# Kernel optimization log

Measured on AMD Instinct MI355X. Metric: run time of the kernel, lower is better.

The kernel has to match this reference:

```python
import jax, jax.numpy as jnp
import numpy as np

L, d, D, X, B = 64, 2, 32, 2, 2048  # sites, local dim, bond dim, kraus dim, batch
STD = 0.01  # kernel_init = normal(stddev=0.01)


def setup_inputs() -> dict:
    key = jax.random.key(0)
    k1, k2, k3, k4 = jax.random.split(key, 4)
    # local quantum-number indices for (row, col) halves: shape [B, 2L]
    qn = jax.random.randint(k1, (B, 2 * L), 0, d, dtype=jnp.int32)
    # boundary tensors: random + all-ones boundary (as in setup())
    left = STD * jax.random.normal(k2, (d, D, X), jnp.float32) + jnp.ones((d, D, X), jnp.float32)
    right = STD * jax.random.normal(k3, (d, D, X), jnp.float32) + jnp.ones((d, D, X), jnp.float32)
    # middle tensors: random + identity on the (D,D) bond indices for every (site, s, kraus)
    iden = jnp.broadcast_to(jnp.eye(D, dtype=jnp.float32)[None, None, :, :, None], (L - 2, d, D, D, X))
    middle = STD * jax.random.normal(k4, (L - 2, d, D, D, X), jnp.float32) + iden
    return {"qn": qn, "left_tensors": left, "right_tensors": right, "middle_tensors": middle}


def _contract_mpdo(qn, left_tensors, right_tensors, middle_tensors):
    # qn: [2L] ints; split into row / column quantum numbers of the density matrix
    qn_r, qn_c = jnp.split(qn, 2, axis=-1)
    # left/right boundary edges: (D,X) @ (X,D) -> (D,D)
    left_edge = left_tensors[qn_r[0]] @ jnp.conj(left_tensors[qn_c[0]]).T
    right_edge = right_tensors[qn_r[-1]] @ jnp.conj(right_tensors[qn_c[-1]]).T

    @jax.checkpoint
    def step(edge, pair):
        tensor, sr, sc = pair  # tensor: (d,D,D,X)
        # (D,D,X) x (D,D) -> (D,X,D)
        tri = jnp.einsum('ijk,il->jkl', tensor[sr], edge)
        # (D,X,D) x (D,D,X) -> (D,D)
        new_edge = jnp.einsum('jkl,lmk->jm', tri, jnp.conj(tensor[sc]))
        return new_edge, None

    edge, _ = jax.lax.scan(step, left_edge, (middle_tensors, qn_r[1:-1], qn_c[1:-1]), unroll=1)
    return jnp.einsum('ij,ij->', edge, right_edge)


def reference(qn, left_tensors, right_tensors, middle_tensors):
    rho = jax.vmap(lambda q: _contract_mpdo(q, left_tensors, right_tensors, middle_tensors))(qn)
    return jnp.log(rho.astype(jnp.complex64))
```

## Files before the change

### kernel.cpp

```cpp
#include <hip/hip_runtime.h>
#include <hip/hip_bf16.h>
#include <math.h>


typedef __attribute__((ext_vector_type(8)))  short short8;
typedef __attribute__((ext_vector_type(16))) float f32x16;

#define EPITCH 33

static __device__ inline unsigned pk2(float lo, float hi) {
    union { __hip_bfloat162 h; unsigned u; } cv;
    cv.h = __float22bfloat162_rn(make_float2(lo, hi));
    return cv.u;
}
static __device__ inline short8 mk8(unsigned u0, unsigned u1, unsigned u2, unsigned u3) {
    union { short8 v; unsigned u[4]; } r;
    r.u[0] = u0; r.u[1] = u1; r.u[2] = u2; r.u[3] = u3;
    return r.v;
}
static __device__ inline void pl32swap(unsigned& x, unsigned& y) {
    asm("v_permlane32_swap_b32 %0, %1" : "+v"(x), "+v"(y));
}
static __device__ inline f32x16 MFMA(short8 a, short8 b, f32x16 c) {
    return __builtin_amdgcn_mfma_f32_32x32x16_bf16(a, b, c, 0, 0, 0);
}
static __device__ inline f32x16 zero16() {
    f32x16 z = {0.f,0.f,0.f,0.f,0.f,0.f,0.f,0.f,0.f,0.f,0.f,0.f,0.f,0.f,0.f,0.f};
    return z;
}

__global__ __launch_bounds__(256, 2) void mpdo_mfma(
    const int*   __restrict__ qn,
    const float* __restrict__ left,
    const float* __restrict__ right,
    const float* __restrict__ middle,
    float*       __restrict__ out,
    const int    cplx)
{
    __shared__ unsigned mid_b[2048];
    __shared__ float    E_s[4][32*EPITCH];

    const int t    = threadIdx.x;
    const int w    = t >> 6;
    const int lane = t & 63;
    const int hi   = lane >> 5;
    const int col  = lane & 31;
    const int elem = blockIdx.x * 4 + w;
    const int* q   = qn + (size_t)elem * 128;
    float* Ew = E_s[w];

    const int sp = (t >> 4) & 15;
    const int sj = t & 15;
    const int jj = sj * 2;
    const float dj = (sp == sj) ? 1.0f : 0.0f;
    const int v0 = (0 + 2*sp) * 16 + sj;
    const int v1 = (32 + 2*sp) * 16 + sj;

    int rowr[16];
    #pragma unroll
    for (int r = 0; r < 16; ++r) rowr[r] = (r & 3) + 8*(r >> 2) + 4*hi;

    float e[16];
    {
        const float* Lr = left + (size_t)q[0]  * 64;
        const float* Lc = left + (size_t)q[64] * 64;
        const float c0v = Lc[col*2 + 0], c1v = Lc[col*2 + 1];
        #pragma unroll
        for (int r = 0; r < 16; ++r)
            e[r] = Lr[rowr[r]*2 + 0] * c0v + Lr[rowr[r]*2 + 1] * c1v;
    }

    const float4* gm = (const float4*)middle;
    float4 A0 = gm[v0], A1 = gm[v0 + 16], B0 = gm[v1], B1 = gm[v1 + 16];
    int srn = q[1], scn = q[65];

    for (int site = 1; site <= 62; ++site) {
        {
            uint2* m2 = (uint2*)mid_b;
            m2[((0*16 + sp)*32 + jj) >> 1] = make_uint2(pk2(A0.x - dj, A1.x), pk2(A0.z, A1.z - dj));
            m2[((1*16 + sp)*32 + jj) >> 1] = make_uint2(pk2(A0.y - dj, A1.y), pk2(A0.w, A1.w - dj));
            m2[((2*16 + sp)*32 + jj) >> 1] = make_uint2(pk2(B0.x - dj, B1.x), pk2(B0.z, B1.z - dj));
            m2[((3*16 + sp)*32 + jj) >> 1] = make_uint2(pk2(B0.y - dj, B1.y), pk2(B0.w, B1.w - dj));
        }
        #pragma unroll
        for (int r = 0; r < 16; ++r) Ew[rowr[r]*EPITCH + col] = e[r];
        __syncthreads();

        const int sr = srn, sc = scn;
        if (site < 62) {
            const float4* gn = (const float4*)(middle + (size_t)site * 4096);
            A0 = gn[v0]; A1 = gn[v0 + 16]; B0 = gn[v1]; B1 = gn[v1 + 16];
            srn = q[site + 1]; scn = q[site + 65];
        }

        short8 aT[2][2], bF[2][2];
        #pragma unroll
        for (int k = 0; k < 2; ++k) {
            #pragma unroll
            for (int h = 0; h < 2; ++h) {
                const int pa = ((sr*2 + k)*16 + 8*h + 4*hi) * 32 + col;
                aT[k][h] = mk8(mid_b[pa], mid_b[pa+32], mid_b[pa+64], mid_b[pa+96]);
                const int pb = ((sc*2 + k)*16 + 8*h + 4*hi) * 32 + col;
                bF[k][h] = mk8(mid_b[pb], mid_b[pb+32], mid_b[pb+64], mid_b[pb+96]);
            }
        }
        short8 EA[2];
        #pragma unroll
        for (int h = 0; h < 2; ++h) {
            const int base = col*EPITCH + 16*h + 8*hi;
            const float f0 = Ew[base+0], f1 = Ew[base+1], f2 = Ew[base+2], f3 = Ew[base+3];
            const float f4 = Ew[base+4], f5 = Ew[base+5], f6 = Ew[base+6], f7 = Ew[base+7];
            EA[h] = mk8(pk2(f0,f1), pk2(f2,f3), pk2(f4,f5), pk2(f6,f7));
        }
        short8 EB[2];
        #pragma unroll
        for (int h = 0; h < 2; ++h) {
            unsigned ua = pk2(e[8*h+0], e[8*h+1]);
            unsigned ub = pk2(e[8*h+2], e[8*h+3]);
            unsigned uc = pk2(e[8*h+4], e[8*h+5]);
            unsigned ud = pk2(e[8*h+6], e[8*h+7]);
            pl32swap(ua, uc); pl32swap(ub, ud);
            EB[h] = mk8(ua, ub, uc, ud);
        }

        f32x16 V0 = MFMA(EA[0], bF[0][0], zero16());
        V0 = MFMA(EA[1], bF[0][1], V0);
        f32x16 V1 = MFMA(EA[0], bF[1][0], zero16());
        V1 = MFMA(EA[1], bF[1][1], V1);
        f32x16 acc = MFMA(aT[0][0], EB[0], zero16());
        acc = MFMA(aT[0][1], EB[1], acc);
        acc = MFMA(aT[1][0], EB[0], acc);
        acc = MFMA(aT[1][1], EB[1], acc);
        #pragma unroll
        for (int k = 0; k < 2; ++k) {
            const f32x16& V = k ? V1 : V0;
            #pragma unroll
            for (int h = 0; h < 2; ++h) {
                unsigned ua = pk2(V[8*h+0], V[8*h+1]);
                unsigned ub = pk2(V[8*h+2], V[8*h+3]);
                unsigned uc = pk2(V[8*h+4], V[8*h+5]);
                unsigned ud = pk2(V[8*h+6], V[8*h+7]);
                pl32swap(ua, uc); pl32swap(ub, ud);
                acc = MFMA(aT[k][h], mk8(ua, ub, uc, ud), acc);
            }
        }
        #pragma unroll
        for (int r = 0; r < 16; ++r)
            e[r] = 2.0f*e[r] + acc[r] + V0[r] + V1[r];
        __syncthreads();
    }

    {
        const float* Rr = right + (size_t)q[63]  * 64;
        const float* Rc = right + (size_t)q[127] * 64;
        const float rc0 = Rc[col*2 + 0], rc1 = Rc[col*2 + 1];
        float part = 0.f;
        #pragma unroll
        for (int r = 0; r < 16; ++r) {
            const float re = Rr[rowr[r]*2 + 0]*rc0 + Rr[rowr[r]*2 + 1]*rc1;
            part += e[r] * re;
        }
        #pragma unroll
        for (int off = 32; off > 0; off >>= 1)
            part += __shfl_down(part, off, 64);
        if (lane == 0) {
            const float re = logf(fabsf(part));
            if (cplx) {
                out[2*elem + 0] = re;
                out[2*elem + 1] = (part < 0.f) ? 3.14159265358979323846f : 0.f;
            } else {
                out[elem] = re;
            }
        }
    }
}

extern "C" void kernel_launch(void* const* d_in, const int* in_sizes, int n_in,
                              void* d_out, int out_size, void* d_ws, size_t ws_size,
                              hipStream_t stream) {
    const int*   qn     = (const int*)  d_in[0];
    const float* left   = (const float*)d_in[1];
    const float* right  = (const float*)d_in[2];
    const float* middle = (const float*)d_in[3];
    float* out = (float*)d_out;

    const int B    = in_sizes[0] / 128;
    const int cplx = (out_size >= 2 * B) ? 1 : 0;
    mpdo_mfma<<<B / 4, 256, 0, stream>>>(qn, left, right, middle, out, cplx);
}
```

Baseline: 142.2 us.

## Split each MPDO chain across two waves by Kraus index and exchange partial sums

Each batch element is now handled by two wavefronts, each owning one Kraus index k, instead of one wavefront doing both. Each wave does half the MFMAs per site. The two waves exchange their bf16-packed partial contributions through shared memory after a block barrier, and launch bounds rise to 4 blocks per CU to raise occupancy. The aim is to shorten the serial per-site latency chain and double the wave count. The cost is extra LDS traffic, extra bf16 rounding of the partial sums, and twice as many blocks.

After: 213.4 us. +50.0%, slower.

```diff
diff --git a/kernel.cpp b/kernel.cpp
--- a/kernel.cpp
+++ b/kernel.cpp
@@ -29,7 +29,7 @@
     return z;
 }
 
-__global__ __launch_bounds__(256, 2) void mpdo_mfma(
+__global__ __launch_bounds__(256, 4) void mpdo_mfma2(
     const int*   __restrict__ qn,
     const float* __restrict__ left,
     const float* __restrict__ right,
@@ -38,16 +38,19 @@
     const int    cplx)
 {
     __shared__ unsigned mid_b[2048];
-    __shared__ float    E_s[4][32*EPITCH];
+    __shared__ float    E_s[2][32*EPITCH];
+    __shared__ unsigned cbuf[4][512];
 
     const int t    = threadIdx.x;
     const int w    = t >> 6;
     const int lane = t & 63;
     const int hi   = lane >> 5;
     const int col  = lane & 31;
-    const int elem = blockIdx.x * 4 + w;
+    const int ew   = w >> 1;
+    const int kw   = w & 1;
+    const int elem = blockIdx.x * 2 + ew;
     const int* q   = qn + (size_t)elem * 128;
-    float* Ew = E_s[w];
+    float* Ew = E_s[ew];
 
     const int sp = (t >> 4) & 15;
     const int sj = t & 15;
@@ -59,6 +62,9 @@
     int rowr[16];
     #pragma unroll
     for (int r = 0; r < 16; ++r) rowr[r] = (r & 3) + 8*(r >> 2) + 4*hi;
+    int rpidx[8];
+    #pragma unroll
+    for (int r = 0; r < 8; ++r) rpidx[r] = (r & 1) + 2*hi + 4*(r >> 1);
 
     float e[16];
     {
@@ -93,16 +99,13 @@
             srn = q[site + 1]; scn = q[site + 65];
         }
 
-        short8 aT[2][2], bF[2][2];
-        #pragma unroll
-        for (int k = 0; k < 2; ++k) {
-            #pragma unroll
-            for (int h = 0; h < 2; ++h) {
-                const int pa = ((sr*2 + k)*16 + 8*h + 4*hi) * 32 + col;
-                aT[k][h] = mk8(mid_b[pa], mid_b[pa+32], mid_b[pa+64], mid_b[pa+96]);
-                const int pb = ((sc*2 + k)*16 + 8*h + 4*hi) * 32 + col;
-                bF[k][h] = mk8(mid_b[pb], mid_b[pb+32], mid_b[pb+64], mid_b[pb+96]);
-            }
+        short8 aT[2], bF[2];
+        #pragma unroll
+        for (int h = 0; h < 2; ++h) {
+            const int pa = ((sr*2 + kw)*16 + 8*h + 4*hi) * 32 + col;
+            aT[h] = mk8(mid_b[pa], mid_b[pa+32], mid_b[pa+64], mid_b[pa+96]);
+            const int pb = ((sc*2 + kw)*16 + 8*h + 4*hi) * 32 + col;
+            bF[h] = mk8(mid_b[pb], mid_b[pb+32], mid_b[pb+64], mid_b[pb+96]);
         }
         short8 EA[2];
         #pragma unroll
@@ -123,17 +126,11 @@
             EB[h] = mk8(ua, ub, uc, ud);
         }
 
-        f32x16 V0 = MFMA(EA[0], bF[0][0], zero16());
-        V0 = MFMA(EA[1], bF[0][1], V0);
-        f32x16 V1 = MFMA(EA[0], bF[1][0], zero16());
-        V1 = MFMA(EA[1], bF[1][1], V1);
-        f32x16 acc = MFMA(aT[0][0], EB[0], zero16());
-        acc = MFMA(aT[0][1], EB[1], acc);
-        acc = MFMA(aT[1][0], EB[0], acc);
-        acc = MFMA(aT[1][1], EB[1], acc);
-        #pragma unroll
-        for (int k = 0; k < 2; ++k) {
-            const f32x16& V = k ? V1 : V0;
+        f32x16 V = MFMA(EA[0], bF[0], zero16());
+        V = MFMA(EA[1], bF[1], V);
+        f32x16 acc = MFMA(aT[0], EB[0], zero16());
+        acc = MFMA(aT[1], EB[1], acc);
+        {
             #pragma unroll
             for (int h = 0; h < 2; ++h) {
                 unsigned ua = pk2(V[8*h+0], V[8*h+1]);
@@ -141,13 +138,37 @@
                 unsigned uc = pk2(V[8*h+4], V[8*h+5]);
                 unsigned ud = pk2(V[8*h+6], V[8*h+7]);
                 pl32swap(ua, uc); pl32swap(ub, ud);
-                acc = MFMA(aT[k][h], mk8(ua, ub, uc, ud), acc);
+                acc = MFMA(aT[h], mk8(ua, ub, uc, ud), acc);
             }
         }
-        #pragma unroll
-        for (int r = 0; r < 16; ++r)
-            e[r] = 2.0f*e[r] + acc[r] + V0[r] + V1[r];
+
+        unsigned cp[8];
+        #pragma unroll
+        for (int r = 0; r < 8; ++r) {
+            cp[r] = pk2(acc[2*r] + V[2*r], acc[2*r+1] + V[2*r+1]);
+            cbuf[w][rpidx[r]*32 + col] = cp[r];
+        }
         __syncthreads();
+
+        {
+            const unsigned* pbuf = &cbuf[w ^ 1][0];
+            #pragma unroll
+            for (int r = 0; r < 8; ++r) {
+                const unsigned uo = cp[r];
+                const unsigned up = pbuf[rpidx[r]*32 + col];
+                const float o0 = __uint_as_float(uo << 16);
+                const float o1 = __uint_as_float(uo & 0xffff0000u);
+                const float p0 = __uint_as_float(up << 16);
+                const float p1 = __uint_as_float(up & 0xffff0000u);
+                if (kw == 0) {
+                    e[2*r]   = fmaf(2.f, e[2*r],   o0) + p0;
+                    e[2*r+1] = fmaf(2.f, e[2*r+1], o1) + p1;
+                } else {
+                    e[2*r]   = fmaf(2.f, e[2*r],   p0) + o0;
+                    e[2*r+1] = fmaf(2.f, e[2*r+1], p1) + o1;
+                }
+            }
+        }
     }
 
     {
@@ -163,7 +184,7 @@
         #pragma unroll
         for (int off = 32; off > 0; off >>= 1)
             part += __shfl_down(part, off, 64);
-        if (lane == 0) {
+        if (lane == 0 && kw == 0) {
             const float re = logf(fabsf(part));
             if (cplx) {
                 out[2*elem + 0] = re;
@@ -186,5 +207,5 @@
 
     const int B    = in_sizes[0] / 128;
     const int cplx = (out_size >= 2 * B) ? 1 : 0;
-    mpdo_mfma<<<B / 4, 256, 0, stream>>>(qn, left, right, middle, out, cplx);
-}
+    mpdo_mfma2<<<B / 2, 256, 0, stream>>>(qn, left, right, middle, out, cplx);
+}
```

## Prestage middle tensors as bf16 MFMA fragments in workspace, drop block syncs

Applied to the files above, without the earlier changes.

A new prestage kernel converts the middle tensors to bf16 once per call, with the identity already subtracted, and lays them out in the exact MFMA operand order in the workspace. The main kernel then loads per-lane fragments for the selected sr/sc slices straight from global memory, prefetching one site ahead. This removes the per-site shared-memory staging of the whole middle tensor and both __syncthreads, since each wave now only uses its own LDS edge buffer. The site loop is also unrolled by two with ping-pong registers. The cost is a second launch plus more gathered global loads per wave, and the old kernel is kept as a fallback when the workspace is too small.

Result: faster. 129.2 us (-9.1%).

```diff
diff --git a/kernel.cpp b/kernel.cpp
--- a/kernel.cpp
+++ b/kernel.cpp
@@ -18,6 +18,9 @@
     r.u[0] = u0; r.u[1] = u1; r.u[2] = u2; r.u[3] = u3;
     return r.v;
 }
+static __device__ inline short8 S8(uint4 u) {
+    union { uint4 a; short8 v; } c; c.a = u; return c.v;
+}
 static __device__ inline void pl32swap(unsigned& x, unsigned& y) {
     asm("v_permlane32_swap_b32 %0, %1" : "+v"(x), "+v"(y));
 }
@@ -29,16 +32,120 @@
     return z;
 }
 
-__global__ __launch_bounds__(256, 2) void mpdo_mfma(
-    const int*   __restrict__ qn,
-    const float* __restrict__ left,
-    const float* __restrict__ right,
-    const float* __restrict__ middle,
-    float*       __restrict__ out,
-    const int    cplx)
+__global__ __launch_bounds__(256) void mpdo_prestage(
+    const float* __restrict__ middle, unsigned* __restrict__ ws)
 {
-    __shared__ unsigned mid_b[2048];
-    __shared__ float    E_s[4][32*EPITCH];
+    const int site = blockIdx.x;
+    const int t    = threadIdx.x;
+    const int s    = t >> 7;
+    const int h    = (t >> 6) & 1;
+    const int hi   = (t >> 5) & 1;
+    const int col  = t & 31;
+    const float2* m2 = (const float2*)middle + (size_t)(site*2 + s) * 1024;
+    float2 v[8];
+    #pragma unroll
+    for (int e = 0; e < 8; ++e) {
+        const int kk = 16*h + 8*hi + e;
+        float2 d = m2[kk*32 + col];
+        if (kk == col) { d.x -= 1.f; d.y -= 1.f; }
+        v[e] = d;
+    }
+    uint4 o0, o1;
+    o0.x = pk2(v[0].x, v[1].x); o0.y = pk2(v[2].x, v[3].x);
+    o0.z = pk2(v[4].x, v[5].x); o0.w = pk2(v[6].x, v[7].x);
+    o1.x = pk2(v[0].y, v[1].y); o1.y = pk2(v[2].y, v[3].y);
+    o1.z = pk2(v[4].y, v[5].y); o1.w = pk2(v[6].y, v[7].y);
+    uint4* w4 = (uint4*)ws;
+    const int lane_off = hi*32 + col;
+    w4[((site*2 + s)*4 + 0 + h)*64 + lane_off] = o0;
+    w4[((site*2 + s)*4 + 2 + h)*64 + lane_off] = o1;
+}
+
+#define SITE_BODY(CA, CB, NA, NB, SITE)                                          \
+  {                                                                              \
+        \
+    float ef[16];                                                                \
+    _Pragma("unroll")                                                            \
+    for (int h = 0; h < 2; ++h) {                                                \
+      const int base = col*EPITCH + 16*h + 8*hi;                                 \
+      _Pragma("unroll")                                                          \
+      for (int c = 0; c < 8; ++c) ef[h*8 + c] = Ew[base + c];                    \
+    }                                                                            \
+                                                  \
+    short8 EB[2];                                                                \
+    _Pragma("unroll")                                                            \
+    for (int h = 0; h < 2; ++h) {                                                \
+      unsigned ua = pk2(e[8*h+0], e[8*h+1]);                                     \
+      unsigned ub = pk2(e[8*h+2], e[8*h+3]);                                     \
+      unsigned uc = pk2(e[8*h+4], e[8*h+5]);                                     \
+      unsigned ud = pk2(e[8*h+6], e[8*h+7]);                                     \
+      pl32swap(ua, uc); pl32swap(ub, ud);                                        \
+      EB[h] = mk8(ua, ub, uc, ud);                                               \
+    }                                                                            \
+                                                              \
+    f32x16 acc0 = MFMA(S8(CA[0]), EB[0], zero16());                              \
+    acc0 = MFMA(S8(CA[1]), EB[1], acc0);                                         \
+    f32x16 acc1 = MFMA(S8(CA[2]), EB[0], zero16());                              \
+    acc1 = MFMA(S8(CA[3]), EB[1], acc1);                                         \
+                                                                    \
+    short8 EA[2];                                                                \
+    _Pragma("unroll")                                                            \
+    for (int h = 0; h < 2; ++h)                                                  \
+      EA[h] = mk8(pk2(ef[8*h+0], ef[8*h+1]), pk2(ef[8*h+2], ef[8*h+3]),          \
+                  pk2(ef[8*h+4], ef[8*h+5]), pk2(ef[8*h+6], ef[8*h+7]));         \
+                                                                \
+    f32x16 V0 = MFMA(EA[0], S8(CB[0]), zero16());                                \
+    V0 = MFMA(EA[1], S8(CB[1]), V0);                                             \
+    f32x16 V1 = MFMA(EA[0], S8(CB[2]), zero16());                                \
+    V1 = MFMA(EA[1], S8(CB[3]), V1);                                             \
+                            \
+    {                                                                            \
+      const int pfi = ((SITE) < 62) ? (SITE) : 61;                               \
+      const int ba = (pfi*2 + srn)*4, bb = (pfi*2 + scn)*4;                      \
+      _Pragma("unroll")                                                          \
+      for (int kh = 0; kh < 4; ++kh) {                                           \
+        NA[kh] = w4g[(ba + kh)*64 + lane_off];                                   \
+        NB[kh] = w4g[(bb + kh)*64 + lane_off];                                   \
+      }                                                                          \
+      const int qi = ((SITE) + 2 <= 62) ? (SITE) + 2 : 62;                       \
+      srn = q[qi]; scn = q[qi + 64];                                             \
+    }                                                                            \
+                                             \
+    _Pragma("unroll")                                                            \
+    for (int h = 0; h < 2; ++h) {                                                \
+      unsigned ua = pk2(V0[8*h+0], V0[8*h+1]);                                   \
+      unsigned ub = pk2(V0[8*h+2], V0[8*h+3]);                                   \
+      unsigned uc = pk2(V0[8*h+4], V0[8*h+5]);                                   \
+      unsigned ud = pk2(V0[8*h+6], V0[8*h+7]);                                   \
+      pl32swap(ua, uc); pl32swap(ub, ud);                                        \
+      acc0 = MFMA(S8(CA[h]), mk8(ua, ub, uc, ud), acc0);                         \
+    }                                                                            \
+    _Pragma("unroll")                                                            \
+    for (int h = 0; h < 2; ++h) {                                                \
+      unsigned ua = pk2(V1[8*h+0], V1[8*h+1]);                                   \
+      unsigned ub = pk2(V1[8*h+2], V1[8*h+3]);                                   \
+      unsigned uc = pk2(V1[8*h+4], V1[8*h+5]);                                   \
+      unsigned ud = pk2(V1[8*h+6], V1[8*h+7]);                                   \
+      pl32swap(ua, uc); pl32swap(ub, ud);                                        \
+      acc1 = MFMA(S8(CA[2+h]), mk8(ua, ub, uc, ud), acc1);                       \
+    }                                                                            \
+          \
+    _Pragma("unroll")                                                            \
+    for (int r = 0; r < 16; ++r)                                                 \
+      e[r] = fmaf(2.f, e[r], (acc0[r] + acc1[r]) + (V0[r] + V1[r]));             \
+    _Pragma("unroll")                                                            \
+    for (int r = 0; r < 16; ++r) Ew[rowr[r]*EPITCH + col] = e[r];                \
+  }
+
+__global__ __launch_bounds__(256, 2) void mpdo_ws(
+    const int*      __restrict__ qn,
+    const float*    __restrict__ left,
+    const float*    __restrict__ right,
+    const unsigned* __restrict__ ws,
+    float*          __restrict__ out,
+    const int       cplx)
+{
+    __shared__ float E_all[4][32*EPITCH];
 
     const int t    = threadIdx.x;
     const int w    = t >> 6;
@@ -47,14 +154,9 @@
     const int col  = lane & 31;
     const int elem = blockIdx.x * 4 + w;
     const int* q   = qn + (size_t)elem * 128;
-    float* Ew = E_s[w];
-
-    const int sp = (t >> 4) & 15;
-    const int sj = t & 15;
-    const int jj = sj * 2;
-    const float dj = (sp == sj) ? 1.0f : 0.0f;
-    const int v0 = (0 + 2*sp) * 16 + sj;
-    const int v1 = (32 + 2*sp) * 16 + sj;
+    float* Ew = E_all[w];
+    const int lane_off = hi*32 + col;
+    const uint4* w4g = (const uint4*)ws;
 
     int rowr[16];
     #pragma unroll
@@ -69,7 +171,83 @@
         for (int r = 0; r < 16; ++r)
             e[r] = Lr[rowr[r]*2 + 0] * c0v + Lr[rowr[r]*2 + 1] * c1v;
     }
-
+    #pragma unroll
+    for (int r = 0; r < 16; ++r) Ew[rowr[r]*EPITCH + col] = e[r];
+
+    uint4 CA[4], CB[4], NA[4], NB[4];
+    {
+        const int sr = q[1], sc = q[65];
+        const int ba = sr*4, bb = sc*4;
+        #pragma unroll
+        for (int kh = 0; kh < 4; ++kh) {
+            CA[kh] = w4g[(ba + kh)*64 + lane_off];
+            CB[kh] = w4g[(bb + kh)*64 + lane_off];
+        }
+    }
+    int srn = q[2], scn = q[66];
+
+    #pragma unroll 1
+    for (int it = 0; it < 31; ++it) {
+        const int siteA = 2*it + 1;
+        SITE_BODY(CA, CB, NA, NB, siteA)
+        SITE_BODY(NA, NB, CA, CB, siteA + 1)
+    }
+
+    {
+        const float* Rr = right + (size_t)q[63]  * 64;
+        const float* Rc = right + (size_t)q[127] * 64;
+        const float rc0 = Rc[col*2 + 0], rc1 = Rc[col*2 + 1];
+        float part = 0.f;
+        #pragma unroll
+        for (int r = 0; r < 16; ++r) {
+            const float re = Rr[rowr[r]*2 + 0]*rc0 + Rr[rowr[r]*2 + 1]*rc1;
+            part += e[r] * re;
+        }
+        #pragma unroll
+        for (int off = 32; off > 0; off >>= 1)
+            part += __shfl_down(part, off, 64);
+        if (lane == 0) {
+            const float re = logf(fabsf(part));
+            if (cplx) {
+                out[2*elem + 0] = re;
+                out[2*elem + 1] = (part < 0.f) ? 3.14159265358979323846f : 0.f;
+            } else {
+                out[elem] = re;
+            }
+        }
+    }
+}
+
+__global__ __launch_bounds__(256, 2) void mpdo_mfma_fb(
+    const int* __restrict__ qn, const float* __restrict__ left,
+    const float* __restrict__ right, const float* __restrict__ middle,
+    float* __restrict__ out, const int cplx)
+{
+    __shared__ unsigned mid_b[2048];
+    __shared__ float    E_s[4][32*EPITCH];
+
+    const int t = threadIdx.x, w = t >> 6, lane = t & 63;
+    const int hi = lane >> 5, col = lane & 31;
+    const int elem = blockIdx.x * 4 + w;
+    const int* q = qn + (size_t)elem * 128;
+    float* Ew = E_s[w];
+    const int sp = (t >> 4) & 15, sj = t & 15, jj = sj * 2;
+    const float dj = (sp == sj) ? 1.0f : 0.0f;
+    const int v0 = (0 + 2*sp) * 16 + sj, v1 = (32 + 2*sp) * 16 + sj;
+
+    int rowr[16];
+    #pragma unroll
+    for (int r = 0; r < 16; ++r) rowr[r] = (r & 3) + 8*(r >> 2) + 4*hi;
+
+    float e[16];
+    {
+        const float* Lr = left + (size_t)q[0]  * 64;
+        const float* Lc = left + (size_t)q[64] * 64;
+        const float c0v = Lc[col*2 + 0], c1v = Lc[col*2 + 1];
+        #pragma unroll
+        for (int r = 0; r < 16; ++r)
+            e[r] = Lr[rowr[r]*2 + 0] * c0v + Lr[rowr[r]*2 + 1] * c1v;
+    }
     const float4* gm = (const float4*)middle;
     float4 A0 = gm[v0], A1 = gm[v0 + 16], B0 = gm[v1], B1 = gm[v1 + 16];
     int srn = q[1], scn = q[65];
@@ -85,17 +263,15 @@
         #pragma unroll
         for (int r = 0; r < 16; ++r) Ew[rowr[r]*EPITCH + col] = e[r];
         __syncthreads();
-
         const int sr = srn, sc = scn;
         if (site < 62) {
             const float4* gn = (const float4*)(middle + (size_t)site * 4096);
             A0 = gn[v0]; A1 = gn[v0 + 16]; B0 = gn[v1]; B1 = gn[v1 + 16];
             srn = q[site + 1]; scn = q[site + 65];
         }
-
         short8 aT[2][2], bF[2][2];
         #pragma unroll
-        for (int k = 0; k < 2; ++k) {
+        for (int k = 0; k < 2; ++k)
             #pragma unroll
             for (int h = 0; h < 2; ++h) {
                 const int pa = ((sr*2 + k)*16 + 8*h + 4*hi) * 32 + col;
@@ -103,14 +279,12 @@
                 const int pb = ((sc*2 + k)*16 + 8*h + 4*hi) * 32 + col;
                 bF[k][h] = mk8(mid_b[pb], mid_b[pb+32], mid_b[pb+64], mid_b[pb+96]);
             }
-        }
         short8 EA[2];
         #pragma unroll
         for (int h = 0; h < 2; ++h) {
             const int base = col*EPITCH + 16*h + 8*hi;
-            const float f0 = Ew[base+0], f1 = Ew[base+1], f2 = Ew[base+2], f3 = Ew[base+3];
-            const float f4 = Ew[base+4], f5 = Ew[base+5], f6 = Ew[base+6], f7 = Ew[base+7];
-            EA[h] = mk8(pk2(f0,f1), pk2(f2,f3), pk2(f4,f5), pk2(f6,f7));
+            EA[h] = mk8(pk2(Ew[base+0], Ew[base+1]), pk2(Ew[base+2], Ew[base+3]),
+                        pk2(Ew[base+4], Ew[base+5]), pk2(Ew[base+6], Ew[base+7]));
         }
         short8 EB[2];
         #pragma unroll
@@ -122,11 +296,8 @@
             pl32swap(ua, uc); pl32swap(ub, ud);
             EB[h] = mk8(ua, ub, uc, ud);
         }
-
-        f32x16 V0 = MFMA(EA[0], bF[0][0], zero16());
-        V0 = MFMA(EA[1], bF[0][1], V0);
-        f32x16 V1 = MFMA(EA[0], bF[1][0], zero16());
-        V1 = MFMA(EA[1], bF[1][1], V1);
+        f32x16 V0 = MFMA(EA[0], bF[0][0], zero16()); V0 = MFMA(EA[1], bF[0][1], V0);
+        f32x16 V1 = MFMA(EA[0], bF[1][0], zero16()); V1 = MFMA(EA[1], bF[1][1], V1);
         f32x16 acc = MFMA(aT[0][0], EB[0], zero16());
         acc = MFMA(aT[0][1], EB[1], acc);
         acc = MFMA(aT[1][0], EB[0], acc);
@@ -149,28 +320,21 @@
             e[r] = 2.0f*e[r] + acc[r] + V0[r] + V1[r];
         __syncthreads();
     }
-
     {
         const float* Rr = right + (size_t)q[63]  * 64;
         const float* Rc = right + (size_t)q[127] * 64;
         const float rc0 = Rc[col*2 + 0], rc1 = Rc[col*2 + 1];
         float part = 0.f;
         #pragma unroll
-        for (int r = 0; r < 16; ++r) {
-            const float re = Rr[rowr[r]*2 + 0]*rc0 + Rr[rowr[r]*2 + 1]*rc1;
-            part += e[r] * re;
-        }
+        for (int r = 0; r < 16; ++r)
+            part += e[r] * (Rr[rowr[r]*2 + 0]*rc0 + Rr[rowr[r]*2 + 1]*rc1);
         #pragma unroll
         for (int off = 32; off > 0; off >>= 1)
             part += __shfl_down(part, off, 64);
         if (lane == 0) {
             const float re = logf(fabsf(part));
-            if (cplx) {
-                out[2*elem + 0] = re;
-                out[2*elem + 1] = (part < 0.f) ? 3.14159265358979323846f : 0.f;
-            } else {
-                out[elem] = re;
-            }
+            if (cplx) { out[2*elem] = re; out[2*elem+1] = (part < 0.f) ? 3.14159265f : 0.f; }
+            else      { out[elem] = re; }
         }
     }
 }
@@ -186,5 +350,13 @@
 
     const int B    = in_sizes[0] / 128;
     const int cplx = (out_size >= 2 * B) ? 1 : 0;
-    mpdo_mfma<<<B / 4, 256, 0, stream>>>(qn, left, right, middle, out, cplx);
-}
+    const size_t need = 62ull * 8192ull;
+
+    if (ws_size >= need) {
+        mpdo_prestage<<<62, 256, 0, stream>>>(middle, (unsigned*)d_ws);
+        mpdo_ws<<<B / 4, 256, 0, stream>>>(qn, left, right, (const unsigned*)d_ws,
+                                           out, cplx);
+    } else {
+        mpdo_mfma_fb<<<B / 4, 256, 0, stream>>>(qn, left, right, middle, out, cplx);
+    }
+}
```
